# Performance work log

Measured on AMD Instinct MI355X. Metric: run time of the kernel, lower is better.

## Reference

```python
import jax, jax.numpy as jnp
import numpy as np

D_MODEL = 256
D_STATE = 64
HEADDIM = 64
EXPAND = 2
D_INNER = EXPAND * D_MODEL        # 512
D_SSM = D_INNER                   # 512
NGROUPS = 1
NHEADS = D_SSM // HEADDIM         # 8
CONV_DIM = D_SSM + 2 * NGROUPS * D_STATE   # 640
D_IN_PROJ = 2 * D_INNER + 2 * NGROUPS * D_STATE + NHEADS  # 1160
BATCH, Himg, Wimg = 8, 64, 64
EPS = 1e-5


def causal_dw_conv1d(x, w, b):
    """Depthwise causal conv1d + SiLU. x:(B,C,L), w:(C,K), b:(C,)"""
    K = w.shape[1]
    L = x.shape[-1]
    xp = jnp.pad(x, ((0, 0), (0, 0), (K - 1, 0)))
    y = b[None, :, None]
    for k in range(K):
        y = y + w[:, k][None, :, None] * xp[:, :, k:k + L]
    return jax.nn.silu(y)


def setup_inputs() -> dict:
    key = jax.random.key(0)
    ks = jax.random.split(key, 12)
    u = jax.random.normal(ks[0], (BATCH, D_MODEL, Himg, Wimg), jnp.float32)
    in_proj_w = jax.random.normal(ks[1], (D_IN_PROJ, D_MODEL), jnp.float32) * 0.02
    conv_dt_w = jax.random.normal(ks[2], (NHEADS, 4), jnp.float32) * 0.1
    # dt_bias via inverse-softplus of dt ~ logU(1e-3, 0.1) as in the module init
    dt0 = jnp.exp(jax.random.uniform(ks[3], (NHEADS,)) * (np.log(0.1) - np.log(0.001)) + np.log(0.001))
    dt_bias = dt0 + jnp.log(-jnp.expm1(-dt0))
    conv_xBC_w = jax.random.normal(ks[4], (CONV_DIM, 3), jnp.float32) * 0.1
    conv_xBC_b = jax.random.normal(ks[5], (CONV_DIM,), jnp.float32) * 0.02
    conv_z_w = jax.random.normal(ks[6], (D_SSM, 3), jnp.float32) * 0.1
    conv_z_b = jax.random.normal(ks[7], (D_SSM,), jnp.float32) * 0.02
    A_log = jnp.log(jax.random.uniform(ks[8], (NHEADS,), minval=1.0, maxval=16.0))
    D_param = jnp.ones((NHEADS,), jnp.float32)
    norm_w = jnp.ones((D_SSM,), jnp.float32)
    out_proj_w = jax.random.normal(ks[9], (D_MODEL, D_SSM, 3, 3), jnp.float32) * 0.02
    return {"u": u, "in_proj_w": in_proj_w, "conv_dt_w": conv_dt_w, "dt_bias": dt_bias,
            "conv_xBC_w": conv_xBC_w, "conv_xBC_b": conv_xBC_b,
            "conv_z_w": conv_z_w, "conv_z_b": conv_z_b,
            "A_log": A_log, "D_param": D_param, "norm_w": norm_w, "out_proj_w": out_proj_w}


def reference(u, in_proj_w, conv_dt_w, dt_bias, conv_xBC_w, conv_xBC_b,
              conv_z_w, conv_z_b, A_log, D_param, norm_w, out_proj_w):
    B, C, H, W = u.shape
    L = H * W
    # 1x1 conv in_proj -> (B, D_IN_PROJ, L)
    zxbcdt = jnp.einsum('oc,bchw->bohw', in_proj_w, u).reshape(B, D_IN_PROJ, L)
    z = zxbcdt[:, :D_SSM]                                  # (B, D_SSM, L)
    xBC = zxbcdt[:, D_SSM:D_SSM + CONV_DIM]                # (B, CONV_DIM, L)
    dt = zxbcdt[:, D_SSM + CONV_DIM:]                      # (B, NHEADS, L)

    A = -jnp.exp(A_log)                                    # (NHEADS,)
    dt = causal_dw_conv1d(dt, conv_dt_w, dt_bias)          # (B, H, L), silu'd
    xBC = causal_dw_conv1d(xBC, conv_xBC_w, conv_xBC_b)    # (B, CONV_DIM, L)

    x = xBC[:, :D_SSM]                                     # (B, D_SSM, L)
    Bm = jnp.transpose(xBC[:, D_SSM:D_SSM + D_STATE], (0, 2, 1))   # (B, L, N)
    Cm = jnp.transpose(xBC[:, D_SSM + D_STATE:], (0, 2, 1))        # (B, L, N)

    # x: (B, h*c, L) -> V: (B, h, L, c)
    V = jnp.transpose(x.reshape(B, NHEADS, HEADDIM, L), (0, 1, 3, 2))
    # dA = dt * A per head: (B, h, L, 1)
    dA = dt[:, :, :, None] * A[None, :, None, None]
    V_scaled = V * dA
    # non-causal linear attention duality (ngroups==1)
    KV = jnp.einsum('bln,bhld->bhnd', Bm, V_scaled)        # (B, h, N, d)
    y = jnp.einsum('bln,bhnd->bhld', Cm, KV) + V * D_param[None, :, None, None]
    y = jnp.transpose(y, (0, 2, 1, 3)).reshape(B, L, D_SSM)

    # gate branch
    zc = causal_dw_conv1d(z, conv_z_w, conv_z_b)           # (B, D_SSM, L)
    zc = jnp.transpose(zc, (0, 2, 1))                      # (B, L, D_SSM)
    # RMSNormGated, norm_before_gate=False: gate first then normalize
    yg = y * jax.nn.silu(zc)
    yn = yg * jax.lax.rsqrt(jnp.mean(yg * yg, axis=-1, keepdims=True) + EPS) * norm_w

    y_img = jnp.transpose(yn, (0, 2, 1)).reshape(B, D_SSM, H, W)
    out = jax.lax.conv_general_dilated(y_img, out_proj_w, (1, 1), 'SAME',
                                       dimension_numbers=('NCHW', 'OIHW', 'NCHW'))
    return out
```

## Files before the change

### kernel.cpp

```cpp
#include <hip/hip_runtime.h>
#include <math.h>


constexpr int BATCH  = 8;
constexpr int CIN    = 256;
constexpr int HH     = 64, WW = 64;
constexpr int L      = HH * WW;
constexpr int DPROJ  = 1160;
constexpr int DSSM   = 512;
constexpr int DSTATE = 64;
constexpr int NH     = 8;
constexpr int HD     = 64;
constexpr int CONVD  = 640;
constexpr int COUT   = 256;
constexpr float EPS  = 1e-5f;

typedef __attribute__((ext_vector_type(8))) short short8;
typedef __attribute__((ext_vector_type(4))) float f32x4;

static __device__ __forceinline__ float silu_f(float x) {
    return x / (1.f + __expf(-x));
}
static __device__ __forceinline__ float bf2f(unsigned short u) {
    return __uint_as_float(((unsigned)u) << 16);
}
static __device__ __forceinline__ unsigned short f2bf(float f) {
    unsigned x = __float_as_uint(f);
    unsigned r = (x + 0x7FFFu + ((x >> 16) & 1u)) >> 16;
    return (unsigned short)r;
}

static __device__ __forceinline__ void gl2lds16(const unsigned short* g, short* l) {
    __builtin_amdgcn_global_load_lds(
        (const __attribute__((address_space(1))) unsigned int*)g,
        (__attribute__((address_space(3))) unsigned int*)l, 16, 0, 0);
}

__global__ __launch_bounds__(256) void k_wb2(const float* __restrict__ W,
                                             unsigned short* __restrict__ Wt2) {
    int idx8 = blockIdx.x * 256 + threadIdx.x;
    int tile = idx8 >> 9;
    int within = (idx8 & 511) * 8;
    int row = within >> 5;
    int slp = (within >> 3) & 3;
    int oblk = tile >> 3, ks = tile & 7;
    int o = oblk * 128 + row;
    int c = ks * 32 + (slp ^ (row & 3)) * 8;
    unsigned short s[8] = {0, 0, 0, 0, 0, 0, 0, 0};
    if (o < DPROJ) {
        float4 v0 = *(const float4*)(W + (size_t)o * CIN + c);
        float4 v1 = *(const float4*)(W + (size_t)o * CIN + c + 4);
        s[0] = f2bf(v0.x); s[1] = f2bf(v0.y); s[2] = f2bf(v0.z); s[3] = f2bf(v0.w);
        s[4] = f2bf(v1.x); s[5] = f2bf(v1.y); s[6] = f2bf(v1.z); s[7] = f2bf(v1.w);
    }
    *(uint4*)(Wt2 + (size_t)tile * 4096 + within) = *(uint4*)s;
}

__global__ __launch_bounds__(256) void k_uT(const float* __restrict__ u,
                                            unsigned short* __restrict__ uTt) {
    __shared__ float Ts[32][33];
    int l0 = blockIdx.x * 32;
    int c0 = blockIdx.y * 32;
    int b  = blockIdx.z;
    int tid = threadIdx.x;
    {
        int r = tid >> 3, c4 = tid & 7;
        float4 v = *(const float4*)(u + ((size_t)b * CIN + c0 + r) * L + l0 + c4 * 4);
        Ts[r][c4 * 4 + 0] = v.x;
        Ts[r][c4 * 4 + 1] = v.y;
        Ts[r][c4 * 4 + 2] = v.z;
        Ts[r][c4 * 4 + 3] = v.w;
    }
    __syncthreads();
    {
        int lr = tid >> 3, cg = tid & 7;
        unsigned short s[4];
#pragma unroll
        for (int j = 0; j < 4; ++j) s[j] = f2bf(Ts[cg * 4 + j][lr]);
        int lg = l0 + lr;
        int tile = ((b * 32 + (lg >> 7)) << 3) + (c0 >> 5);
        int row = lg & 127;
        int slot = (cg >> 1) ^ (row & 3);
        size_t off = (size_t)tile * 4096 + row * 32 + slot * 8 + (cg & 1) * 4;
        *(uint2*)(uTt + off) = *(uint2*)s;
    }
}

__global__ __launch_bounds__(256) void k_wprep(const float* __restrict__ Wt,
                                               unsigned short* __restrict__ Wb2) {
    int i = blockIdx.x * 256 + threadIdx.x;
    int co = i >> 9, ci = i & 511;
    const float* src = Wt + (size_t)i * 9;
#pragma unroll
    for (int tap = 0; tap < 9; ++tap) {
        Wb2[(((size_t)tap * 64 + (ci >> 3)) * 256 + co) * 8 + (ci & 7)] = f2bf(src[tap]);
    }
}

__global__ __launch_bounds__(256) void k_inprojm(const unsigned short* __restrict__ Wt2,
                                                 const unsigned short* __restrict__ uTt,
                                                 unsigned short* __restrict__ zx) {
    __shared__ short Ab[2][4096];
    __shared__ short Bbuf[2][4096];
    int lblk = blockIdx.x, oblk = blockIdx.y, b = blockIdx.z;
    int tid = threadIdx.x, lane = tid & 63, w = tid >> 6;
    int laneN = lane & 15, laneK = lane >> 4;

    const unsigned short* At = uTt + (size_t)(b * 32 + lblk) * 8 * 4096;
    const unsigned short* Bt = Wt2 + (size_t)oblk * 8 * 4096;

    f32x4 acc[4][4];
#pragma unroll
    for (int mt = 0; mt < 4; ++mt)
#pragma unroll
        for (int nt = 0; nt < 4; ++nt) acc[mt][nt] = (f32x4){0.f, 0.f, 0.f, 0.f};

    gl2lds16(At + tid * 8,        &Ab[0][tid * 8]);
    gl2lds16(At + 2048 + tid * 8, &Ab[0][2048 + tid * 8]);
    gl2lds16(Bt + tid * 8,        &Bbuf[0][tid * 8]);
    gl2lds16(Bt + 2048 + tid * 8, &Bbuf[0][2048 + tid * 8]);
    __syncthreads();

    int arow = (w & 1) * 64;
    int brow = (w >> 1) * 64;
    int asl = (laneK ^ (laneN & 3)) * 8;

    int cur = 0;
    for (int ks = 0; ks < 8; ++ks) {
        if (ks < 7) {
            const unsigned short* an = At + (size_t)(ks + 1) * 4096;
            const unsigned short* bn = Bt + (size_t)(ks + 1) * 4096;
            int c2 = cur ^ 1;
            gl2lds16(an + tid * 8,        &Ab[c2][tid * 8]);
            gl2lds16(an + 2048 + tid * 8, &Ab[c2][2048 + tid * 8]);
            gl2lds16(bn + tid * 8,        &Bbuf[c2][tid * 8]);
            gl2lds16(bn + 2048 + tid * 8, &Bbuf[c2][2048 + tid * 8]);
        }
        short8 av[4], bv[4];
#pragma unroll
        for (int mt = 0; mt < 4; ++mt)
            av[mt] = *(const short8*)&Ab[cur][(arow + mt * 16 + laneN) * 32 + asl];
#pragma unroll
        for (int nt = 0; nt < 4; ++nt)
            bv[nt] = *(const short8*)&Bbuf[cur][(brow + nt * 16 + laneN) * 32 + asl];
#pragma unroll
        for (int mt = 0; mt < 4; ++mt)
#pragma unroll
            for (int nt = 0; nt < 4; ++nt)
                acc[mt][nt] = __builtin_amdgcn_mfma_f32_16x16x32_bf16(av[mt], bv[nt], acc[mt][nt], 0, 0, 0);
        __syncthreads();
        cur ^= 1;
    }

    unsigned short* zb = zx + (size_t)b * DPROJ * L;
    int lbase = lblk * 128 + arow;
#pragma unroll
    for (int nt = 0; nt < 4; ++nt) {
        int o = oblk * 128 + brow + nt * 16 + laneN;
        if (o < DPROJ) {
#pragma unroll
            for (int mt = 0; mt < 4; ++mt) {
                unsigned short s[4] = {f2bf(acc[mt][nt].x), f2bf(acc[mt][nt].y),
                                       f2bf(acc[mt][nt].z), f2bf(acc[mt][nt].w)};
                *(uint2*)(zb + (size_t)o * L + lbase + mt * 16 + laneK * 4) = *(uint2*)s;
            }
        }
    }
}

__global__ __launch_bounds__(256) void k_dtdA(const unsigned short* __restrict__ zx,
                                              const float* __restrict__ cw,
                                              const float* __restrict__ cb,
                                              const float* __restrict__ Alog,
                                              float* __restrict__ dA) {
    int idx = blockIdx.x * 256 + threadIdx.x;
    int l = idx & (L - 1);
    int h = (idx >> 12) & (NH - 1);
    int b = idx >> 15;
    const unsigned short* row = zx + ((size_t)b * DPROJ + DSSM + CONVD + h) * L;
    float y = cb[h];
#pragma unroll
    for (int k = 0; k < 4; ++k) {
        int ls = l + k - 3;
        if (ls >= 0) y += cw[h * 4 + k] * bf2f(row[ls]);
    }
    dA[idx] = silu_f(y) * (-__expf(Alog[h]));
}

__global__ __launch_bounds__(256) void k_xbc(const unsigned short* __restrict__ zx,
                                             const float* __restrict__ cw,
                                             const float* __restrict__ cb,
                                             unsigned short* __restrict__ xbc) {
    int idx = blockIdx.x * 256 + threadIdx.x;
    int lg = idx & (L / 8 - 1);
    int c  = (idx >> 9) % CONVD;
    int b  = idx / (CONVD * (L / 8));
    int l0 = lg * 8;
    const unsigned short* row = zx + ((size_t)b * DPROJ + DSSM + c) * L;
    float x[10];
    uint4 raw = *(const uint4*)(row + l0);
    const unsigned short* s = (const unsigned short*)&raw;
#pragma unroll
    for (int t = 0; t < 8; ++t) x[2 + t] = bf2f(s[t]);
    if (l0 > 0) { x[0] = bf2f(row[l0 - 2]); x[1] = bf2f(row[l0 - 1]); }
    else        { x[0] = 0.f; x[1] = 0.f; }
    float w0 = cw[c * 3 + 0], w1 = cw[c * 3 + 1], w2 = cw[c * 3 + 2], bb = cb[c];
    uint4 o;
    unsigned short* os = (unsigned short*)&o;
#pragma unroll
    for (int t = 0; t < 8; ++t) {
        float y = bb + w0 * x[t] + w1 * x[t + 1] + w2 * x[t + 2];
        os[t] = f2bf(silu_f(y));
    }
    *(uint4*)(xbc + ((size_t)b * CONVD + c) * L + l0) = o;
}

__global__ __launch_bounds__(256) void k_kvm(const unsigned short* __restrict__ xbc,
                                             const float* __restrict__ dA,
                                             float* __restrict__ pKV) {
    __shared__ float red[4][4096];
    int kc = blockIdx.x, h = blockIdx.y, b = blockIdx.z;
    int tid = threadIdx.x, lane = tid & 63, w = tid >> 6;
    int laneN = lane & 15, laneK = lane >> 4;

    const unsigned short* Bb = xbc + ((size_t)b * CONVD + DSSM) * L;
    const unsigned short* Vb = xbc + ((size_t)b * CONVD + h * HD) * L;
    const float* dAp = dA + ((size_t)b * NH + h) * L;

    f32x4 acc[4][4];
#pragma unroll
    for (int mt = 0; mt < 4; ++mt)
#pragma unroll
        for (int nt = 0; nt < 4; ++nt) acc[mt][nt] = (f32x4){0.f, 0.f, 0.f, 0.f};

    int kbase = kc * 512 + w * 128;
#pragma unroll
    for (int ks = 0; ks < 4; ++ks) {
        int kl = kbase + ks * 32 + laneK * 8;
        float4 da0 = *(const float4*)(dAp + kl);
        float4 da1 = *(const float4*)(dAp + kl + 4);
        float dav[8] = {da0.x, da0.y, da0.z, da0.w, da1.x, da1.y, da1.z, da1.w};
        short8 afr[4];
#pragma unroll
        for (int mt = 0; mt < 4; ++mt) {
            uint4 raw = *(const uint4*)(Bb + (size_t)(mt * 16 + laneN) * L + kl);
            const unsigned short* s = (const unsigned short*)&raw;
            short8 af;
#pragma unroll
            for (int j = 0; j < 8; ++j) af[j] = (short)f2bf(bf2f(s[j]) * dav[j]);
            afr[mt] = af;
        }
#pragma unroll
        for (int nt = 0; nt < 4; ++nt) {
            short8 bfr = *(const short8*)(Vb + (size_t)(nt * 16 + laneN) * L + kl);
#pragma unroll
            for (int mt = 0; mt < 4; ++mt)
                acc[mt][nt] = __builtin_amdgcn_mfma_f32_16x16x32_bf16(afr[mt], bfr, acc[mt][nt], 0, 0, 0);
        }
    }

#pragma unroll
    for (int mt = 0; mt < 4; ++mt)
#pragma unroll
        for (int nt = 0; nt < 4; ++nt)
#pragma unroll
            for (int j = 0; j < 4; ++j)
                red[w][(mt * 16 + laneK * 4 + j) * 64 + nt * 16 + laneN] = acc[mt][nt][j];
    __syncthreads();

    float* dst = pKV + (((size_t)(b * NH + h) * 8 + kc) * 4096);
#pragma unroll
    for (int q = 0; q < 4; ++q) {
        int off = q * 1024 + tid * 4;
        float4 s0 = *(const float4*)&red[0][off];
        float4 s1 = *(const float4*)&red[1][off];
        float4 s2 = *(const float4*)&red[2][off];
        float4 s3 = *(const float4*)&red[3][off];
        float4 r;
        r.x = s0.x + s1.x + s2.x + s3.x;
        r.y = s0.y + s1.y + s2.y + s3.y;
        r.z = s0.z + s1.z + s2.z + s3.z;
        r.w = s0.w + s1.w + s2.w + s3.w;
        *(float4*)(dst + off) = r;
    }
}

__global__ __launch_bounds__(256) void k_kvred(const float* __restrict__ pKV,
                                               float* __restrict__ KV) {
    int flat4 = blockIdx.x * 256 + threadIdx.x;
    int bh = flat4 >> 10;
    int nd = (flat4 & 1023) * 4;
    float4 r = make_float4(0.f, 0.f, 0.f, 0.f);
#pragma unroll
    for (int kc = 0; kc < 8; ++kc) {
        float4 v = *(const float4*)(pKV + ((size_t)bh * 8 + kc) * 4096 + nd);
        r.x += v.x; r.y += v.y; r.z += v.z; r.w += v.w;
    }
    *(float4*)(KV + (size_t)bh * 4096 + nd) = r;
}

constexpr int Y_LT = 128;

__global__ __launch_bounds__(256) void k_y5a(const unsigned short* __restrict__ xbc,
                                             const unsigned short* __restrict__ zx,
                                             const float* __restrict__ KV,
                                             const float* __restrict__ zw,
                                             const float* __restrict__ zb,
                                             const float* __restrict__ Dp,
                                             unsigned short* __restrict__ ygout) {
    __shared__ float Cs[DSTATE][Y_LT + 4];
    __shared__ float KVs[DSTATE][HD + 4];
    int l0 = blockIdx.x * Y_LT;
    int h  = blockIdx.y;
    int b  = blockIdx.z;
    int tid = threadIdx.x;
    int td = tid >> 4, tl = tid & 15;

    const unsigned short* xb = xbc + (size_t)b * CONVD * L;
#pragma unroll
    for (int j = 0; j < 4; ++j) {
        int i = j * 256 + tid;
        int nn = i >> 4, c8 = i & 15;
        uint4 raw = *(const uint4*)(xb + (size_t)(DSSM + DSTATE + nn) * L + l0 + c8 * 8);
        const unsigned short* s = (const unsigned short*)&raw;
#pragma unroll
        for (int t = 0; t < 8; ++t) Cs[nn][c8 * 8 + t] = bf2f(s[t]);
    }
    const float* kvb = KV + ((size_t)b * NH + h) * DSTATE * HD;
#pragma unroll
    for (int j = 0; j < 4; ++j) {
        int i = j * 256 + tid;
        int nn = i >> 4, d4 = i & 15;
        *(float4*)&KVs[nn][d4 * 4] = *(const float4*)(kvb + (size_t)nn * HD + d4 * 4);
    }
    __syncthreads();

    float acc[4][8];
#pragma unroll
    for (int i = 0; i < 4; ++i)
#pragma unroll
        for (int j = 0; j < 8; ++j) acc[i][j] = 0.f;

    for (int nn = 0; nn < DSTATE; ++nn) {
        float4 kv = *(const float4*)&KVs[nn][td * 4];
        float cl[8];
        *(float4*)&cl[0] = *(const float4*)&Cs[nn][tl * 8];
        *(float4*)&cl[4] = *(const float4*)&Cs[nn][tl * 8 + 4];
#pragma unroll
        for (int j = 0; j < 8; ++j) {
            acc[0][j] += kv.x * cl[j];
            acc[1][j] += kv.y * cl[j];
            acc[2][j] += kv.z * cl[j];
            acc[3][j] += kv.w * cl[j];
        }
    }

    float Dh = Dp[h];
    int lbase = l0 + tl * 8;
#pragma unroll
    for (int dj = 0; dj < 4; ++dj) {
        int c = h * HD + td * 4 + dj;
        float v[8];
        {
            uint4 raw = *(const uint4*)(xb + (size_t)c * L + lbase);
            const unsigned short* s = (const unsigned short*)&raw;
#pragma unroll
            for (int t = 0; t < 8; ++t) v[t] = bf2f(s[t]);
        }
        const unsigned short* zrow = zx + ((size_t)b * DPROJ + c) * L;
        float zv[12];
        if (lbase >= 4) {
            uint2 z0 = *(const uint2*)(zrow + lbase - 4);
            const unsigned short* s = (const unsigned short*)&z0;
#pragma unroll
            for (int t = 0; t < 4; ++t) zv[t] = bf2f(s[t]);
        } else {
            zv[0] = zv[1] = zv[2] = zv[3] = 0.f;
        }
        {
            uint4 z1 = *(const uint4*)(zrow + lbase);
            const unsigned short* s = (const unsigned short*)&z1;
#pragma unroll
            for (int t = 0; t < 8; ++t) zv[4 + t] = bf2f(s[t]);
        }
        float w0 = zw[c * 3 + 0], w1 = zw[c * 3 + 1], w2 = zw[c * 3 + 2];
        float bz = zb[c];
        uint4 pk;
        unsigned short* sp = (unsigned short*)&pk;
#pragma unroll
        for (int lj = 0; lj < 8; ++lj) {
            float y = acc[dj][lj] + v[lj] * Dh;
            float zy = bz + w0 * zv[lj + 2] + w1 * zv[lj + 3] + w2 * zv[lj + 4];
            sp[lj] = f2bf(y * silu_f(silu_f(zy)));
        }
        *(uint4*)(ygout + (size_t)b * DPROJ * L + (size_t)c * L + lbase) = pk;
    }
}

constexpr int R_LT = 32;

__global__ __launch_bounds__(256) void k_y5bT(const unsigned short* __restrict__ yg,
                                              const float* __restrict__ nw,
                                              unsigned short* __restrict__ ynT) {
    __shared__ float ygs[DSSM][R_LT + 1];
    __shared__ float red[8][R_LT];
    __shared__ float rs[R_LT];
    int l0 = blockIdx.x * R_LT;
    int b  = blockIdx.y;
    int tid = threadIdx.x;
    int ll = tid & 31, grp = tid >> 5;
    const unsigned short* ygb = yg + (size_t)b * DPROJ * L;
#pragma unroll
    for (int j = 0; j < 64; ++j) {
        int i = j * 256 + tid;
        int c = i >> 5, lc = i & 31;
        ygs[c][lc] = bf2f(ygb[(size_t)c * L + l0 + lc]);
    }
    __syncthreads();
    float ss = 0.f;
#pragma unroll
    for (int ci = 0; ci < 64; ++ci) {
        float t = ygs[grp * 64 + ci][ll];
        ss += t * t;
    }
    red[grp][ll] = ss;
    __syncthreads();
    if (tid < R_LT) {
        float s = 0.f;
#pragma unroll
        for (int g = 0; g < 8; ++g) s += red[g][tid];
        rs[tid] = rsqrtf(s * (1.f / DSSM) + EPS);
    }
    __syncthreads();
    int lc = tid & 31, cg = tid >> 5;
    float r = rs[lc];
    unsigned short* dst = ynT + ((size_t)b * L + l0 + lc) * DSSM + cg * 64;
#pragma unroll
    for (int j = 0; j < 8; ++j) {
        uint4 pk;
        unsigned short* sp = (unsigned short*)&pk;
#pragma unroll
        for (int t = 0; t < 8; ++t) {
            int c = cg * 64 + j * 8 + t;
            sp[t] = f2bf(ygs[c][lc] * r * nw[c]);
        }
        *(uint4*)(dst + j * 8) = pk;
    }
}

__global__ __launch_bounds__(256, 4) void k_conv3m(const unsigned short* __restrict__ ynT,
                                                   const unsigned short* __restrict__ Wb2,
                                                   float* __restrict__ out) {
    __shared__ short Alds[4 * 66 * 72];
    int h0  = blockIdx.x * 2;
    int co0 = blockIdx.y * 64;
    int b   = blockIdx.z;
    int tid  = threadIdx.x;
    int lane = tid & 63;
    int wid  = tid >> 6;
    int wm = wid >> 1, wn = wid & 1;
    int laneN = lane & 15, laneK = lane >> 4;

    f32x4 acc[4][2];
#pragma unroll
    for (int mt = 0; mt < 4; ++mt)
#pragma unroll
        for (int nt = 0; nt < 2; ++nt) acc[mt][nt] = (f32x4){0.f, 0.f, 0.f, 0.f};

    const unsigned short* ynb = ynT + (size_t)b * L * DSSM;

    const int a_wi1 = tid >> 2, a_sl = tid & 3;

    if (tid < 64) {
        int rw = tid >> 3, q = tid & 7;
        int r = rw >> 1, wi = (rw & 1) ? 65 : 0;
        *(uint4*)&Alds[(r * 66 + wi) * 72 + q * 8] = make_uint4(0u, 0u, 0u, 0u);
    }

    uint4 pA[8];
#pragma unroll
    for (int j = 0; j < 4; ++j) {
        int hrow = h0 - 1 + j;
        bool ok = (hrow >= 0 && hrow < HH);
        const unsigned short* src = ynb + (size_t)(hrow * WW + a_wi1) * DSSM;
#pragma unroll
        for (int s2 = 0; s2 < 2; ++s2) {
            pA[j * 2 + s2] = make_uint4(0u, 0u, 0u, 0u);
            if (ok) pA[j * 2 + s2] = *(const uint4*)(src + (a_sl + s2 * 4) * 8);
        }
    }

    const unsigned short* wbp =
        Wb2 + ((size_t)laneK * 256 + co0 + wn * 32 + laneN) * 8;

    for (int ci0 = 0; ci0 < DSSM; ci0 += 64) {
        __syncthreads();
#pragma unroll
        for (int j = 0; j < 4; ++j)
#pragma unroll
            for (int s2 = 0; s2 < 2; ++s2)
                *(uint4*)&Alds[(j * 66 + a_wi1 + 1) * 72 + (a_sl + s2 * 4) * 8] = pA[j * 2 + s2];
        __syncthreads();

        if (ci0 + 64 < DSSM) {
            int cin = ci0 + 64;
#pragma unroll
            for (int j = 0; j < 4; ++j) {
                int hrow = h0 - 1 + j;
                bool ok = (hrow >= 0 && hrow < HH);
                const unsigned short* src = ynb + (size_t)(hrow * WW + a_wi1) * DSSM + cin;
#pragma unroll
                for (int s2 = 0; s2 < 2; ++s2) {
                    pA[j * 2 + s2] = make_uint4(0u, 0u, 0u, 0u);
                    if (ok) pA[j * 2 + s2] = *(const uint4*)(src + (a_sl + s2 * 4) * 8);
                }
            }
        }

        const unsigned short* wbc = wbp + (size_t)(ci0 >> 3) * 2048;
        short8 bC[4];
#pragma unroll
        for (int ks = 0; ks < 2; ++ks)
#pragma unroll
            for (int nt = 0; nt < 2; ++nt)
                bC[ks * 2 + nt] = *(const short8*)(wbc + (size_t)ks * 8192 + nt * 128);
#pragma unroll
        for (int tap = 0; tap < 9; ++tap) {
            short8 bN[4];
#pragma unroll
            for (int q = 0; q < 4; ++q) bN[q] = bC[q];
            if (tap < 8) {
#pragma unroll
                for (int ks = 0; ks < 2; ++ks)
#pragma unroll
                    for (int nt = 0; nt < 2; ++nt)
                        bN[ks * 2 + nt] = *(const short8*)(wbc + (size_t)(tap + 1) * 131072 +
                                                          (size_t)ks * 8192 + nt * 128);
            }
            const int kh = tap / 3, kw = tap % 3;
#pragma unroll
            for (int ks = 0; ks < 2; ++ks) {
#pragma unroll
                for (int mt = 0; mt < 4; ++mt) {
                    short8 af = *(const short8*)&Alds[((wm + kh) * 66 + laneN + mt * 16 + kw) * 72 +
                                                      (laneK + ks * 4) * 8];
                    acc[mt][0] = __builtin_amdgcn_mfma_f32_16x16x32_bf16(af, bC[ks * 2 + 0], acc[mt][0], 0, 0, 0);
                    acc[mt][1] = __builtin_amdgcn_mfma_f32_16x16x32_bf16(af, bC[ks * 2 + 1], acc[mt][1], 0, 0, 0);
                }
            }
#pragma unroll
            for (int q = 0; q < 4; ++q) bC[q] = bN[q];
        }
    }

    float* ob = out + (size_t)b * COUT * L + (size_t)(h0 + wm) * WW;
#pragma unroll
    for (int mt = 0; mt < 4; ++mt) {
#pragma unroll
        for (int nt = 0; nt < 2; ++nt) {
            int co = co0 + wn * 32 + nt * 16 + laneN;
            float4 v = make_float4(acc[mt][nt].x, acc[mt][nt].y, acc[mt][nt].z, acc[mt][nt].w);
            *(float4*)(ob + (size_t)co * L + mt * 16 + laneK * 4) = v;
        }
    }
}

extern "C" void kernel_launch(void* const* d_in, const int* in_sizes, int n_in,
                              void* d_out, int out_size, void* d_ws, size_t ws_size,
                              hipStream_t stream) {
    const float* u          = (const float*)d_in[0];
    const float* in_proj_w  = (const float*)d_in[1];
    const float* conv_dt_w  = (const float*)d_in[2];
    const float* dt_bias    = (const float*)d_in[3];
    const float* conv_xBC_w = (const float*)d_in[4];
    const float* conv_xBC_b = (const float*)d_in[5];
    const float* conv_z_w   = (const float*)d_in[6];
    const float* conv_z_b   = (const float*)d_in[7];
    const float* A_log      = (const float*)d_in[8];
    const float* D_param    = (const float*)d_in[9];
    const float* norm_w     = (const float*)d_in[10];
    const float* out_w      = (const float*)d_in[11];
    float* out = (float*)d_out;

    const size_t n_zx  = (size_t)BATCH * DPROJ * L;
    const size_t n_xbc = (size_t)BATCH * CONVD * L;
    const size_t n_yn  = (size_t)BATCH * DSSM * L;
    const size_t n_dA  = (size_t)BATCH * NH * L;
    const size_t n_KV  = (size_t)BATCH * NH * DSTATE * HD;
    const size_t n_pKV = (size_t)BATCH * NH * 8 * DSTATE * HD;
    const size_t n_Wb2 = (size_t)9 * 64 * 256 * 8;
    const size_t need  = 2 * (n_zx + n_xbc + n_yn + n_Wb2) + 4 * (n_dA + n_KV + n_pKV);
    if (ws_size < need) return;

    unsigned short* zx  = (unsigned short*)d_ws;
    unsigned short* xbc = zx + n_zx;
    unsigned short* ynT = xbc + n_xbc;
    float*          dAb = (float*)(ynT + n_yn);
    float*          KV  = dAb + n_dA;
    float*          pKV = KV + n_KV;
    unsigned short* Wb2 = (unsigned short*)(pKV + n_pKV);
    unsigned short* uTt  = ynT;
    unsigned short* Wt2  = (unsigned short*)pKV;
    unsigned short* ygbuf = zx + (size_t)DSSM * L;

    k_wb2<<<160, 256, 0, stream>>>(in_proj_w, Wt2);

    dim3 gt(L / 32, CIN / 32, BATCH);
    k_uT<<<gt, 256, 0, stream>>>(u, uTt);

    k_wprep<<<(COUT * DSSM) / 256, 256, 0, stream>>>(out_w, Wb2);

    dim3 g1(L / 128, 10, BATCH);
    k_inprojm<<<g1, 256, 0, stream>>>(Wt2, uTt, zx);

    k_dtdA<<<BATCH * NH * L / 256, 256, 0, stream>>>(zx, conv_dt_w, dt_bias, A_log, dAb);

    k_xbc<<<BATCH * CONVD * (L / 8) / 256, 256, 0, stream>>>(zx, conv_xBC_w, conv_xBC_b, xbc);

    dim3 g4(8, NH, BATCH);
    k_kvm<<<g4, 256, 0, stream>>>(xbc, dAb, pKV);
    k_kvred<<<256, 256, 0, stream>>>(pKV, KV);

    dim3 g5(L / Y_LT, NH, BATCH);
    k_y5a<<<g5, 256, 0, stream>>>(xbc, zx, KV, conv_z_w, conv_z_b, D_param, ygbuf);

    dim3 g5b(L / R_LT, BATCH);
    k_y5bT<<<g5b, 256, 0, stream>>>(ygbuf, norm_w, ynT);

    dim3 g6(HH / 2, COUT / 64, BATCH);
    k_conv3m<<<g6, 256, 0, stream>>>(ynT, Wb2, out);
}
```

Before: 247.6 us.

## Compute C·KV with bf16 MFMA using pre-transposed C and KV buffers

Replaces the scalar FP32 shared-memory outer-product loop in the y computation with bf16 MFMA 16x16x32 instructions. Two new kernels transpose C into an L-major layout and convert KV into a transposed bf16 buffer, so the operands can be loaded straight from global memory as MFMA fragments. The gating epilogue is reworked to fit the MFMA output layout, which now uses narrower 4-element stores. This costs two extra launches and extra workspace traffic, and quantizing KV to bf16 loses some precision.

```diff
diff --git a/kernel.cpp b/kernel.cpp
--- a/kernel.cpp
+++ b/kernel.cpp
@@ -215,6 +215,30 @@
     *(uint4*)(xbc + ((size_t)b * CONVD + c) * L + l0) = o;
 }
 
+__global__ __launch_bounds__(256) void k_ct(const unsigned short* __restrict__ xbc,
+                                            unsigned short* __restrict__ CT) {
+    __shared__ short Ts[32][33];
+    int l0 = blockIdx.x * 32;
+    int n0 = blockIdx.y * 32;
+    int b  = blockIdx.z;
+    int tid = threadIdx.x;
+    {
+        int r = tid >> 3, q = tid & 7;
+        uint2 v = *(const uint2*)(xbc + ((size_t)b * CONVD + DSSM + DSTATE + n0 + r) * L + l0 + q * 4);
+        const unsigned short* s = (const unsigned short*)&v;
+#pragma unroll
+        for (int t = 0; t < 4; ++t) Ts[r][q * 4 + t] = (short)s[t];
+    }
+    __syncthreads();
+    {
+        int lr = tid >> 3, qn = tid & 7;
+        unsigned short s[4];
+#pragma unroll
+        for (int t = 0; t < 4; ++t) s[t] = (unsigned short)Ts[qn * 4 + t][lr];
+        *(uint2*)(CT + ((size_t)b * L + l0 + lr) * DSTATE + n0 + qn * 4) = *(uint2*)s;
+    }
+}
+
 __global__ __launch_bounds__(256) void k_kvm(const unsigned short* __restrict__ xbc,
                                              const float* __restrict__ dA,
                                              float* __restrict__ pKV) {
@@ -299,101 +323,115 @@
     *(float4*)(KV + (size_t)bh * 4096 + nd) = r;
 }
 
-constexpr int Y_LT = 128;
-
-__global__ __launch_bounds__(256) void k_y5a(const unsigned short* __restrict__ xbc,
-                                             const unsigned short* __restrict__ zx,
-                                             const float* __restrict__ KV,
-                                             const float* __restrict__ zw,
-                                             const float* __restrict__ zb,
-                                             const float* __restrict__ Dp,
-                                             unsigned short* __restrict__ ygout) {
-    __shared__ float Cs[DSTATE][Y_LT + 4];
-    __shared__ float KVs[DSTATE][HD + 4];
-    int l0 = blockIdx.x * Y_LT;
+__global__ __launch_bounds__(256) void k_kvT(const float* __restrict__ KV,
+                                             unsigned short* __restrict__ KVt) {
+    __shared__ float Ts[64][65];
+    int bh = blockIdx.x;
+    int tid = threadIdx.x;
+    const float* src = KV + (size_t)bh * 4096;
+#pragma unroll
+    for (int j = 0; j < 16; ++j) {
+        int idx = j * 256 + tid;
+        Ts[idx >> 6][idx & 63] = src[idx];
+    }
+    __syncthreads();
+    unsigned short* dst = KVt + (size_t)bh * 4096;
+#pragma unroll
+    for (int j = 0; j < 4; ++j) {
+        int idx = j * 256 + tid;
+        int d = idx >> 4, q = idx & 15;
+        unsigned short s[4];
+#pragma unroll
+        for (int t = 0; t < 4; ++t) s[t] = f2bf(Ts[q * 4 + t][d]);
+        *(uint2*)(dst + d * 64 + q * 4) = *(uint2*)s;
+    }
+}
+
+__global__ __launch_bounds__(256) void k_y5am(const unsigned short* __restrict__ CT,
+                                              const unsigned short* __restrict__ KVt,
+                                              const unsigned short* __restrict__ xbc,
+                                              const unsigned short* __restrict__ zx,
+                                              const float* __restrict__ zw,
+                                              const float* __restrict__ zb,
+                                              const float* __restrict__ Dp,
+                                              unsigned short* __restrict__ ygout) {
+    int l0 = blockIdx.x * 128;
     int h  = blockIdx.y;
     int b  = blockIdx.z;
-    int tid = threadIdx.x;
-    int td = tid >> 4, tl = tid & 15;
+    int tid = threadIdx.x, lane = tid & 63, w = tid >> 6;
+    int laneN = lane & 15, laneK = lane >> 4;
+    int lw = l0 + w * 32;
+
+    const unsigned short* ctb = CT + (size_t)b * L * DSTATE;
+    const unsigned short* kvb = KVt + ((size_t)b * NH + h) * HD * DSTATE;
+
+    f32x4 acc[2][4];
+#pragma unroll
+    for (int mt = 0; mt < 2; ++mt)
+#pragma unroll
+        for (int nt = 0; nt < 4; ++nt) acc[mt][nt] = (f32x4){0.f, 0.f, 0.f, 0.f};
+
+#pragma unroll
+    for (int ks = 0; ks < 2; ++ks) {
+        int ko = ks * 32 + laneK * 8;
+        short8 av[2], bv[4];
+#pragma unroll
+        for (int mt = 0; mt < 2; ++mt)
+            av[mt] = *(const short8*)(ctb + (size_t)(lw + mt * 16 + laneN) * DSTATE + ko);
+#pragma unroll
+        for (int nt = 0; nt < 4; ++nt)
+            bv[nt] = *(const short8*)(kvb + (size_t)(nt * 16 + laneN) * DSTATE + ko);
+#pragma unroll
+        for (int mt = 0; mt < 2; ++mt)
+#pragma unroll
+            for (int nt = 0; nt < 4; ++nt)
+                acc[mt][nt] = __builtin_amdgcn_mfma_f32_16x16x32_bf16(av[mt], bv[nt], acc[mt][nt], 0, 0, 0);
+    }
 
     const unsigned short* xb = xbc + (size_t)b * CONVD * L;
-#pragma unroll
-    for (int j = 0; j < 4; ++j) {
-        int i = j * 256 + tid;
-        int nn = i >> 4, c8 = i & 15;
-        uint4 raw = *(const uint4*)(xb + (size_t)(DSSM + DSTATE + nn) * L + l0 + c8 * 8);
-        const unsigned short* s = (const unsigned short*)&raw;
-#pragma unroll
-        for (int t = 0; t < 8; ++t) Cs[nn][c8 * 8 + t] = bf2f(s[t]);
-    }
-    const float* kvb = KV + ((size_t)b * NH + h) * DSTATE * HD;
-#pragma unroll
-    for (int j = 0; j < 4; ++j) {
-        int i = j * 256 + tid;
-        int nn = i >> 4, d4 = i & 15;
-        *(float4*)&KVs[nn][d4 * 4] = *(const float4*)(kvb + (size_t)nn * HD + d4 * 4);
-    }
-    __syncthreads();
-
-    float acc[4][8];
-#pragma unroll
-    for (int i = 0; i < 4; ++i)
-#pragma unroll
-        for (int j = 0; j < 8; ++j) acc[i][j] = 0.f;
-
-    for (int nn = 0; nn < DSTATE; ++nn) {
-        float4 kv = *(const float4*)&KVs[nn][td * 4];
-        float cl[8];
-        *(float4*)&cl[0] = *(const float4*)&Cs[nn][tl * 8];
-        *(float4*)&cl[4] = *(const float4*)&Cs[nn][tl * 8 + 4];
-#pragma unroll
-        for (int j = 0; j < 8; ++j) {
-            acc[0][j] += kv.x * cl[j];
-            acc[1][j] += kv.y * cl[j];
-            acc[2][j] += kv.z * cl[j];
-            acc[3][j] += kv.w * cl[j];
-        }
-    }
-
     float Dh = Dp[h];
-    int lbase = l0 + tl * 8;
-#pragma unroll
-    for (int dj = 0; dj < 4; ++dj) {
-        int c = h * HD + td * 4 + dj;
-        float v[8];
-        {
-            uint4 raw = *(const uint4*)(xb + (size_t)c * L + lbase);
-            const unsigned short* s = (const unsigned short*)&raw;
-#pragma unroll
-            for (int t = 0; t < 8; ++t) v[t] = bf2f(s[t]);
-        }
-        const unsigned short* zrow = zx + ((size_t)b * DPROJ + c) * L;
-        float zv[12];
-        if (lbase >= 4) {
-            uint2 z0 = *(const uint2*)(zrow + lbase - 4);
-            const unsigned short* s = (const unsigned short*)&z0;
-#pragma unroll
-            for (int t = 0; t < 4; ++t) zv[t] = bf2f(s[t]);
-        } else {
-            zv[0] = zv[1] = zv[2] = zv[3] = 0.f;
-        }
-        {
-            uint4 z1 = *(const uint4*)(zrow + lbase);
-            const unsigned short* s = (const unsigned short*)&z1;
-#pragma unroll
-            for (int t = 0; t < 8; ++t) zv[4 + t] = bf2f(s[t]);
-        }
+#pragma unroll
+    for (int nt = 0; nt < 4; ++nt) {
+        int d = nt * 16 + laneN;
+        int c = h * HD + d;
         float w0 = zw[c * 3 + 0], w1 = zw[c * 3 + 1], w2 = zw[c * 3 + 2];
         float bz = zb[c];
-        uint4 pk;
-        unsigned short* sp = (unsigned short*)&pk;
-#pragma unroll
-        for (int lj = 0; lj < 8; ++lj) {
-            float y = acc[dj][lj] + v[lj] * Dh;
-            float zy = bz + w0 * zv[lj + 2] + w1 * zv[lj + 3] + w2 * zv[lj + 4];
-            sp[lj] = f2bf(y * silu_f(silu_f(zy)));
-        }
-        *(uint4*)(ygout + (size_t)b * DPROJ * L + (size_t)c * L + lbase) = pk;
+        const unsigned short* vrow = xb + (size_t)c * L;
+        const unsigned short* zrow = zx + ((size_t)b * DPROJ + c) * L;
+#pragma unroll
+        for (int mt = 0; mt < 2; ++mt) {
+            int lpos = lw + mt * 16 + laneK * 4;
+            float v[4];
+            {
+                uint2 raw = *(const uint2*)(vrow + lpos);
+                const unsigned short* s = (const unsigned short*)&raw;
+#pragma unroll
+                for (int t = 0; t < 4; ++t) v[t] = bf2f(s[t]);
+            }
+            float zv[8];
+            if (lpos >= 4) {
+                uint2 z0 = *(const uint2*)(zrow + lpos - 4);
+                const unsigned short* s = (const unsigned short*)&z0;
+#pragma unroll
+                for (int t = 0; t < 4; ++t) zv[t] = bf2f(s[t]);
+            } else {
+                zv[0] = zv[1] = zv[2] = zv[3] = 0.f;
+            }
+            {
+                uint2 z1 = *(const uint2*)(zrow + lpos);
+                const unsigned short* s = (const unsigned short*)&z1;
+#pragma unroll
+                for (int t = 0; t < 4; ++t) zv[4 + t] = bf2f(s[t]);
+            }
+            unsigned short sp[4];
+#pragma unroll
+            for (int j = 0; j < 4; ++j) {
+                float y = acc[mt][nt][j] + v[j] * Dh;
+                float zy = bz + w0 * zv[j + 2] + w1 * zv[j + 3] + w2 * zv[j + 4];
+                sp[j] = f2bf(y * silu_f(silu_f(zy)));
+            }
+            *(uint2*)(ygout + (size_t)b * DPROJ * L + (size_t)c * L + lpos) = *(uint2*)sp;
+        }
     }
 }
 
@@ -589,7 +627,10 @@
     const size_t n_KV  = (size_t)BATCH * NH * DSTATE * HD;
     const size_t n_pKV = (size_t)BATCH * NH * 8 * DSTATE * HD;
     const size_t n_Wb2 = (size_t)9 * 64 * 256 * 8;
-    const size_t need  = 2 * (n_zx + n_xbc + n_yn + n_Wb2) + 4 * (n_dA + n_KV + n_pKV);
+    const size_t n_ct  = (size_t)BATCH * L * DSTATE;
+    const size_t n_kvt = (size_t)BATCH * NH * HD * DSTATE;
+    const size_t need  = 2 * (n_zx + n_xbc + n_yn + n_Wb2 + n_ct + n_kvt)
+                       + 4 * (n_dA + n_KV + n_pKV);
     if (ws_size < need) return;
 
     unsigned short* zx  = (unsigned short*)d_ws;
@@ -599,6 +640,8 @@
     float*          KV  = dAb + n_dA;
     float*          pKV = KV + n_KV;
     unsigned short* Wb2 = (unsigned short*)(pKV + n_pKV);
+    unsigned short* CT  = Wb2 + n_Wb2;
+    unsigned short* KVt = CT + n_ct;
     unsigned short* uTt  = ynT;
     unsigned short* Wt2  = (unsigned short*)pKV;
     unsigned short* ygbuf = zx + (size_t)DSSM * L;
@@ -617,12 +660,16 @@
 
     k_xbc<<<BATCH * CONVD * (L / 8) / 256, 256, 0, stream>>>(zx, conv_xBC_w, conv_xBC_b, xbc);
 
+    dim3 gct(L / 32, DSTATE / 32, BATCH);
+    k_ct<<<gct, 256, 0, stream>>>(xbc, CT);
+
     dim3 g4(8, NH, BATCH);
     k_kvm<<<g4, 256, 0, stream>>>(xbc, dAb, pKV);
     k_kvred<<<256, 256, 0, stream>>>(pKV, KV);
-
-    dim3 g5(L / Y_LT, NH, BATCH);
-    k_y5a<<<g5, 256, 0, stream>>>(xbc, zx, KV, conv_z_w, conv_z_b, D_param, ygbuf);
+    k_kvT<<<BATCH * NH, 256, 0, stream>>>(KV, KVt);
+
+    dim3 g5(L / 128, NH, BATCH);
+    k_y5am<<<g5, 256, 0, stream>>>(CT, KVt, xbc, zx, conv_z_w, conv_z_b, D_param, ygbuf);
 
     dim3 g5b(L / R_LT, BATCH);
     k_y5bT<<<g5b, 256, 0, stream>>>(ygbuf, norm_w, ynT);
```

New measurement: 248.0 us. About the same (+0.2%).
